# Optimization experiments

Measured on AMD Instinct MI355X. Metric: run time of the kernel, lower is better.

## Reference

```python
import jax, jax.numpy as jnp
import numpy as np

N_NODES = 100000
N_EDGES = 1600000
N_GRAPHS = 64
D_IN, D_HID, D_LAT = 2, 64, 32


def setup_inputs() -> dict:
    key = jax.random.key(0)
    k1, k2, k3, k4, k5, k6, k7 = jax.random.split(key, 7)
    x = jax.random.normal(k1, (N_NODES, D_IN), dtype=jnp.float32)
    edge_index = jax.random.randint(k2, (2, N_EDGES), 0, N_NODES, dtype=jnp.int64)
    batch = jnp.sort(jax.random.randint(k3, (N_NODES,), 0, N_GRAPHS, dtype=jnp.int64))
    # GCNConv params (glorot-ish scale)
    W1 = jax.random.normal(k4, (D_IN, D_HID), dtype=jnp.float32) * (1.0 / np.sqrt(D_IN))
    b1 = jnp.zeros((D_HID,), dtype=jnp.float32)
    W2 = jax.random.normal(k5, (D_HID, D_LAT), dtype=jnp.float32) * (1.0 / np.sqrt(D_HID))
    b2 = jnp.zeros((D_LAT,), dtype=jnp.float32)
    return {"x": x, "W1": W1, "b1": b1, "W2": W2, "b2": b2,
            "edge_index": edge_index, "batch": batch}


def _gcn_conv(x, W, b, src, dst, n_nodes):
    """PyG GCNConv: add self-loops, symmetric deg^-1/2 normalization, linear, scatter-add."""
    h = x @ W  # [N, d_out]
    loop = jnp.arange(n_nodes, dtype=src.dtype)
    src_f = jnp.concatenate([src, loop])
    dst_f = jnp.concatenate([dst, loop])
    deg = jax.ops.segment_sum(jnp.ones_like(dst_f, dtype=h.dtype), dst_f,
                              num_segments=n_nodes)  # in-degree incl. self-loop
    dis = jnp.where(deg > 0, jax.lax.rsqrt(deg), 0.0)
    norm = dis[src_f] * dis[dst_f]  # [E+N]
    msg = h[src_f] * norm[:, None]  # edge gather (memory-bound)
    out = jax.ops.segment_sum(msg, dst_f, num_segments=n_nodes)
    return out + b


def reference(x, W1, b1, W2, b2, edge_index, batch):
    src, dst = edge_index[0], edge_index[1]
    n = x.shape[0]
    h = jax.nn.relu(_gcn_conv(x, W1, b1, src, dst, n))
    z = _gcn_conv(h, W2, b2, src, dst, n)
    # global_mean_pool over graph ids
    sums = jax.ops.segment_sum(z, batch, num_segments=N_GRAPHS)
    cnts = jax.ops.segment_sum(jnp.ones((n,), dtype=z.dtype), batch,
                               num_segments=N_GRAPHS)
    return sums / jnp.maximum(cnts, 1.0)[:, None]
```

## Files before the change

kernel.cpp:

```cpp
#include <hip/hip_runtime.h>
#include <hip/hip_fp16.h>

#define N_NODES  100000
#define N_EDGES  1600000
#define N_GRAPHS 64
#define NBUCK    391
#define NBLK     256
#define CHUNK    (N_EDGES / NBLK)
#define NODEBLK  1563

#define OFF_GSTART 0
#define OFF_ROWPTR 128
#define OFF_DIS    100224
#define OFF_S      200320
#define OFF_CSR    400384
#define OFF_Q      2000384
#define OFF_BHIST  2000384
#define OFF_BOFFL  2100736
#define OFF_BSUM   2201088
#define OFF_BSTART 2201600
#define OFF_TMP    2202112

typedef float fvec2 __attribute__((ext_vector_type(2)));

__device__ __forceinline__ int excl_scan_256(int v, int* wsum) {
  int t = threadIdx.x, lane = t & 63, w = t >> 6;
  int x = v;
#pragma unroll
  for (int off = 1; off < 64; off <<= 1) {
    int y = __shfl_up(x, off, 64);
    if (lane >= off) x += y;
  }
  if (lane == 63) wsum[w] = x;
  __syncthreads();
  if (t == 0) {
    int r = 0;
#pragma unroll
    for (int i = 0; i < 4; ++i) { int tv = wsum[i]; wsum[i] = r; r += tv; }
  }
  __syncthreads();
  return x - v + wsum[w];
}

__device__ __forceinline__ int excl_scan_512(int v, int* wsum) {
  int t = threadIdx.x, lane = t & 63, w = t >> 6;
  int x = v;
#pragma unroll
  for (int off = 1; off < 64; off <<= 1) {
    int y = __shfl_up(x, off, 64);
    if (lane >= off) x += y;
  }
  if (lane == 63) wsum[w] = x;
  __syncthreads();
  if (t == 0) {
    int r = 0;
#pragma unroll
    for (int i = 0; i < 8; ++i) { int tv = wsum[i]; wsum[i] = r; r += tv; }
  }
  __syncthreads();
  return x - v + wsum[w];
}

__global__ void k_hist(const int* __restrict__ dst, int* __restrict__ bhist) {
  __shared__ int hist[NBUCK];
  int t = threadIdx.x, k = blockIdx.x;
  for (int b = t; b < NBUCK; b += 256) hist[b] = 0;
  __syncthreads();
  int e0 = k * CHUNK, e1 = e0 + CHUNK;
  for (int e = e0 + t; e < e1; e += 256) atomicAdd(&hist[dst[e] >> 8], 1);
  __syncthreads();
  for (int b = t; b < NBUCK; b += 256) bhist[b * NBLK + k] = hist[b];
}

__global__ void k_scan_a(const int* __restrict__ bhist, int* __restrict__ boffl,
                         int* __restrict__ bsum, const int* __restrict__ batch,
                         int* __restrict__ gstart) {
  __shared__ int wsum[4];
  int t = threadIdx.x, b = blockIdx.x;
  int i = b * 256 + t;
  if (i < N_NODES) {
    int bi = batch[i];
    if (i == 0) {
      for (int g = 0; g <= bi; ++g) gstart[g] = 0;
    } else {
      int bp = batch[i - 1];
      for (int g = bp + 1; g <= bi; ++g) gstart[g] = i;
    }
    if (i == N_NODES - 1) {
      for (int g = bi + 1; g <= N_GRAPHS; ++g) gstart[g] = N_NODES;
    }
  }
  int v = bhist[b * NBLK + t];
  int ex = excl_scan_256(v, wsum);
  boffl[b * NBLK + t] = ex;
  if (t == NBLK - 1) bsum[b] = ex + v;
}

__global__ void k_scan_b(const int* __restrict__ bsum, int* __restrict__ bstart,
                         float* __restrict__ pooled) {
  __shared__ int wsum[8];
  int t = threadIdx.x;
  for (int i = t; i < N_GRAPHS * 32; i += 512) pooled[i] = 0.f;
  int v = (t < NBUCK) ? bsum[t] : 0;
  int ex = excl_scan_512(v, wsum);
  if (t <= NBUCK) bstart[t] = ex;
}

__global__ void k_scatter(const int* __restrict__ src, const int* __restrict__ dst,
                          const int* __restrict__ bstart, const int* __restrict__ boffl,
                          int* __restrict__ tmp) {
  __shared__ int sbase[NBUCK];
  __shared__ int fill[NBUCK];
  int t = threadIdx.x, k = blockIdx.x;
  for (int b = t; b < NBUCK; b += 256) {
    sbase[b] = bstart[b] + boffl[b * NBLK + k];
    fill[b] = 0;
  }
  __syncthreads();
  int e0 = k * CHUNK, e1 = e0 + CHUNK;
  for (int e = e0 + t; e < e1; e += 256) {
    int s_ = src[e], d_ = dst[e];
    int b = d_ >> 8;
    int pos = sbase[b] + atomicAdd(&fill[b], 1);
    tmp[pos] = (s_ << 8) | (d_ & 255);
  }
}

__global__ void k_fine(const int* __restrict__ tmp, const int* __restrict__ bstart,
                       const float* __restrict__ x, int* __restrict__ csr_src,
                       int* __restrict__ row_ptr, float* __restrict__ dis,
                       float2* __restrict__ s) {
  __shared__ int hist[256];
  __shared__ int fill[256];
  __shared__ int wsum[4];
  int t = threadIdx.x, b = blockIdx.x;
  int base_n = b << 8;
  int e0 = bstart[b], e1 = bstart[b + 1];
  hist[t] = 0;
  __syncthreads();
  for (int e = e0 + t; e < e1; e += 256) atomicAdd(&hist[tmp[e] & 255], 1);
  __syncthreads();
  int h = hist[t];
  int ex = excl_scan_256(h, wsum);
  hist[t] = ex;
  fill[t] = 0;
  int nn = min(256, N_NODES - base_n);
  if (t < nn) {
    int v = base_n + t;
    row_ptr[v] = e0 + ex;
    float dv = rsqrtf((float)(h + 1));
    dis[v] = dv;
    float2 xv = ((const float2*)x)[v];
    s[v] = make_float2(xv.x * dv, xv.y * dv);
  }
  if (b == NBUCK - 1 && t == 0) row_ptr[N_NODES] = e1;
  __syncthreads();
  for (int e = e0 + t; e < e1; e += 256) {
    int p = tmp[e];
    int fine = p & 255;
    int pos = e0 + hist[fine] + atomicAdd(&fill[fine], 1);
    csr_src[pos] = p >> 8;
  }
}

__global__ void __launch_bounds__(64)
k_layer1(const float2* __restrict__ s, const int* __restrict__ row_ptr,
         const int* __restrict__ csr_src, const float* __restrict__ W1,
         const float* __restrict__ b1, const float* __restrict__ W2,
         int4* __restrict__ q8) {
  __shared__ float4 sWB[64];
  __shared__ float4 sW2[512];
  int t = threadIdx.x;
  sWB[t] = make_float4(W1[t], W1[64 + t], b1[t], 0.f);
#pragma unroll
  for (int i = 0; i < 8; ++i) sW2[i * 64 + t] = ((const float4*)W2)[i * 64 + t];
  __syncthreads();
  int base = blockIdx.x * 128;
  int vA = base + t, vB = base + 64 + t;
  bool okA = vA < N_NODES, okB = vB < N_NODES;
  float tA0 = 0.f, tA1 = 0.f, tB0 = 0.f, tB1 = 0.f, dA = 0.f, dB = 0.f;
  if (okA) {
    int beg = row_ptr[vA], end = row_ptr[vA + 1];
    float2 sv = s[vA];
    tA0 = sv.x; tA1 = sv.y;
    int k = beg;
    for (; k + 4 <= end; k += 4) {
      float2 a = s[csr_src[k]], b = s[csr_src[k + 1]];
      float2 c = s[csr_src[k + 2]], d = s[csr_src[k + 3]];
      tA0 += (a.x + b.x) + (c.x + d.x);
      tA1 += (a.y + b.y) + (c.y + d.y);
    }
    for (; k < end; ++k) { float2 su = s[csr_src[k]]; tA0 += su.x; tA1 += su.y; }
    dA = rsqrtf((float)(end - beg + 1));
    tA0 *= dA; tA1 *= dA;
  }
  if (okB) {
    int beg = row_ptr[vB], end = row_ptr[vB + 1];
    float2 sv = s[vB];
    tB0 = sv.x; tB1 = sv.y;
    int k = beg;
    for (; k + 4 <= end; k += 4) {
      float2 a = s[csr_src[k]], b = s[csr_src[k + 1]];
      float2 c = s[csr_src[k + 2]], d = s[csr_src[k + 3]];
      tB0 += (a.x + b.x) + (c.x + d.x);
      tB1 += (a.y + b.y) + (c.y + d.y);
    }
    for (; k < end; ++k) { float2 su = s[csr_src[k]]; tB0 += su.x; tB1 += su.y; }
    dB = rsqrtf((float)(end - beg + 1));
    tB0 *= dB; tB1 *= dB;
  }
  float4 aA[8], aB[8];
#pragma unroll
  for (int m = 0; m < 8; ++m) {
    aA[m] = make_float4(0.f, 0.f, 0.f, 0.f);
    aB[m] = make_float4(0.f, 0.f, 0.f, 0.f);
  }
  for (int j = 0; j < 64; ++j) {
    float4 wb = sWB[j];
    float rA = fmaxf(fmaf(tA0, wb.x, fmaf(tA1, wb.y, wb.z)), 0.f);
    float rB = fmaxf(fmaf(tB0, wb.x, fmaf(tB1, wb.y, wb.z)), 0.f);
#pragma unroll
    for (int m = 0; m < 8; ++m) {
      float4 w = sW2[j * 8 + m];
      aA[m].x = fmaf(rA, w.x, aA[m].x);
      aA[m].y = fmaf(rA, w.y, aA[m].y);
      aA[m].z = fmaf(rA, w.z, aA[m].z);
      aA[m].w = fmaf(rA, w.w, aA[m].w);
      aB[m].x = fmaf(rB, w.x, aB[m].x);
      aB[m].y = fmaf(rB, w.y, aB[m].y);
      aB[m].z = fmaf(rB, w.z, aB[m].z);
      aB[m].w = fmaf(rB, w.w, aB[m].w);
    }
  }
  if (okA) {
    int pk[8];
#pragma unroll
    for (int m = 0; m < 8; ++m) {
      int wrd = __builtin_amdgcn_cvt_pk_fp8_f32(aA[m].x * dA, aA[m].y * dA, 0, false);
      wrd = __builtin_amdgcn_cvt_pk_fp8_f32(aA[m].z * dA, aA[m].w * dA, wrd, true);
      pk[m] = wrd;
    }
    q8[vA * 2]     = make_int4(pk[0], pk[1], pk[2], pk[3]);
    q8[vA * 2 + 1] = make_int4(pk[4], pk[5], pk[6], pk[7]);
  }
  if (okB) {
    int pk[8];
#pragma unroll
    for (int m = 0; m < 8; ++m) {
      int wrd = __builtin_amdgcn_cvt_pk_fp8_f32(aB[m].x * dB, aB[m].y * dB, 0, false);
      wrd = __builtin_amdgcn_cvt_pk_fp8_f32(aB[m].z * dB, aB[m].w * dB, wrd, true);
      pk[m] = wrd;
    }
    q8[vB * 2]     = make_int4(pk[0], pk[1], pk[2], pk[3]);
    q8[vB * 2 + 1] = make_int4(pk[4], pk[5], pk[6], pk[7]);
  }
}

__device__ __forceinline__ float4 qdec(unsigned int d) {
  fvec2 lo = __builtin_amdgcn_cvt_pk_f32_fp8(d, false);
  fvec2 hi = __builtin_amdgcn_cvt_pk_f32_fp8(d, true);
  return make_float4(lo.x, lo.y, hi.x, hi.y);
}

__global__ void k_layer2(const unsigned int* __restrict__ q, const float* __restrict__ dis,
                         const int* __restrict__ row_ptr, const int* __restrict__ csr_src,
                         const int* __restrict__ batch, float* __restrict__ pooled) {
  __shared__ float4 red[32][9];
  int t = threadIdx.x;
  int fp = t & 7;
  int rg = t >> 3;
  int vb = blockIdx.x * 64;
  int nlast = min(vb + 63, N_NODES - 1);
  bool uniform = (batch[vb] == batch[nlast]);
  int v0 = vb + rg * 2;
  int v1 = min(v0 + 2, N_NODES);
  float4 acc = make_float4(0.f, 0.f, 0.f, 0.f);
  int curg = (v0 < N_NODES) ? batch[v0] : -1;
  for (int v = v0; v < v1; ++v) {
    if (!uniform) {
      int g = batch[v];
      if (g != curg) {
        int base = curg * 32 + fp * 4;
        atomicAdd(&pooled[base],     acc.x);
        atomicAdd(&pooled[base + 1], acc.y);
        atomicAdd(&pooled[base + 2], acc.z);
        atomicAdd(&pooled[base + 3], acc.w);
        acc = make_float4(0.f, 0.f, 0.f, 0.f);
        curg = g;
      }
    }
    int e0 = row_ptr[v], e1 = row_ptr[v + 1];
    float4 z = qdec(q[v * 8 + fp]);
    int k = e0;
    for (; k + 8 <= e1; k += 8) {
      int u0 = csr_src[k],     u1 = csr_src[k + 1], u2 = csr_src[k + 2], u3 = csr_src[k + 3];
      int u4 = csr_src[k + 4], u5 = csr_src[k + 5], u6 = csr_src[k + 6], u7 = csr_src[k + 7];
      float4 f0 = qdec(q[u0 * 8 + fp]);
      float4 f1 = qdec(q[u1 * 8 + fp]);
      float4 f2 = qdec(q[u2 * 8 + fp]);
      float4 f3 = qdec(q[u3 * 8 + fp]);
      float4 f4 = qdec(q[u4 * 8 + fp]);
      float4 f5 = qdec(q[u5 * 8 + fp]);
      float4 f6 = qdec(q[u6 * 8 + fp]);
      float4 f7 = qdec(q[u7 * 8 + fp]);
      z.x += ((f0.x + f1.x) + (f2.x + f3.x)) + ((f4.x + f5.x) + (f6.x + f7.x));
      z.y += ((f0.y + f1.y) + (f2.y + f3.y)) + ((f4.y + f5.y) + (f6.y + f7.y));
      z.z += ((f0.z + f1.z) + (f2.z + f3.z)) + ((f4.z + f5.z) + (f6.z + f7.z));
      z.w += ((f0.w + f1.w) + (f2.w + f3.w)) + ((f4.w + f5.w) + (f6.w + f7.w));
    }
    for (; k < e1; ++k) {
      float4 f = qdec(q[csr_src[k] * 8 + fp]);
      z.x += f.x; z.y += f.y; z.z += f.z; z.w += f.w;
    }
    float dvv = dis[v];
    acc.x = fmaf(z.x, dvv, acc.x);
    acc.y = fmaf(z.y, dvv, acc.y);
    acc.z = fmaf(z.z, dvv, acc.z);
    acc.w = fmaf(z.w, dvv, acc.w);
  }
  if (uniform) {
    red[rg][fp] = acc;
    __syncthreads();
    if (t < 8) {
      float4 ssum = make_float4(0.f, 0.f, 0.f, 0.f);
#pragma unroll
      for (int r = 0; r < 32; ++r) {
        float4 x4 = red[r][t];
        ssum.x += x4.x; ssum.y += x4.y; ssum.z += x4.z; ssum.w += x4.w;
      }
      int gg = batch[vb];
      int base = gg * 32 + t * 4;
      atomicAdd(&pooled[base],     ssum.x);
      atomicAdd(&pooled[base + 1], ssum.y);
      atomicAdd(&pooled[base + 2], ssum.z);
      atomicAdd(&pooled[base + 3], ssum.w);
    }
  } else if (v0 < N_NODES) {
    int base = curg * 32 + fp * 4;
    atomicAdd(&pooled[base],     acc.x);
    atomicAdd(&pooled[base + 1], acc.y);
    atomicAdd(&pooled[base + 2], acc.z);
    atomicAdd(&pooled[base + 3], acc.w);
  }
}

__global__ void k_final(float* __restrict__ out, const int* __restrict__ gstart,
                        const float* __restrict__ b2) {
  int i = blockIdx.x * 256 + threadIdx.x;
  if (i < N_GRAPHS * 32) {
    int g = i >> 5, l = i & 31;
    int c = gstart[g + 1] - gstart[g];
    out[i] = (c > 0) ? out[i] / (float)c + b2[l] : 0.f;
  }
}

extern "C" void kernel_launch(void* const* d_in, const int* in_sizes, int n_in,
                              void* d_out, int out_size, void* d_ws, size_t ws_size,
                              hipStream_t stream) {
  (void)in_sizes; (void)n_in; (void)out_size; (void)ws_size;
  const float* x   = (const float*)d_in[0];
  const float* W1  = (const float*)d_in[1];
  const float* b1  = (const float*)d_in[2];
  const float* W2  = (const float*)d_in[3];
  const float* b2  = (const float*)d_in[4];
  const int* edge  = (const int*)d_in[5];
  const int* batch = (const int*)d_in[6];
  const int* src = edge;
  const int* dst = edge + N_EDGES;
  float* out = (float*)d_out;

  int* ws      = (int*)d_ws;
  int* gstart  = ws + OFF_GSTART;
  int* row_ptr = ws + OFF_ROWPTR;
  float* dis   = (float*)(ws + OFF_DIS);
  float2* s    = (float2*)(ws + OFF_S);
  int* csr_src = ws + OFF_CSR;
  int4* q8     = (int4*)(ws + OFF_Q);
  int* bhist   = ws + OFF_BHIST;
  int* boffl   = ws + OFF_BOFFL;
  int* bsum    = ws + OFF_BSUM;
  int* bstart  = ws + OFF_BSTART;
  int* tmp     = ws + OFF_TMP;

  k_hist<<<NBLK, 256, 0, stream>>>(dst, bhist);
  k_scan_a<<<NBUCK, 256, 0, stream>>>(bhist, boffl, bsum, batch, gstart);
  k_scan_b<<<1, 512, 0, stream>>>(bsum, bstart, out);
  k_scatter<<<NBLK, 256, 0, stream>>>(src, dst, bstart, boffl, tmp);
  k_fine<<<NBUCK, 256, 0, stream>>>(tmp, bstart, x, csr_src, row_ptr, dis, s);
  k_layer1<<<(N_NODES + 127) / 128, 64, 0, stream>>>(s, row_ptr, csr_src,
                                                     W1, b1, W2, q8);
  k_layer2<<<NODEBLK, 256, 0, stream>>>((const unsigned int*)q8, dis, row_ptr,
                                        csr_src, batch, out);
  k_final<<<8, 256, 0, stream>>>(out, gstart, b2);
}
```

Baseline: 96.43 us.

## Stage scatter and fine-sort in LDS to coalesce global writes

k_scatter now locally sorts each block's edge chunk into an LDS buffer by bucket, then writes each bucket's contiguous run to global memory. This replaces the random single-int global writes. k_fine likewise loads a bucket's edges into LDS, builds the CSR order in LDS and writes it out contiguously, with a global fallback when a bucket exceeds capacity. Both kernels use more LDS, which lowers occupancy, and the scan helpers gain an extra barrier so wsum can be reused safely.

```diff
diff --git a/kernel.cpp b/kernel.cpp
--- a/kernel.cpp
+++ b/kernel.cpp
@@ -8,6 +8,7 @@
 #define NBLK     256
 #define CHUNK    (N_EDGES / NBLK)
 #define NODEBLK  1563
+#define FCAP     6144
 
 #define OFF_GSTART 0
 #define OFF_ROWPTR 128
@@ -39,7 +40,9 @@
     for (int i = 0; i < 4; ++i) { int tv = wsum[i]; wsum[i] = r; r += tv; }
   }
   __syncthreads();
-  return x - v + wsum[w];
+  int res = x - v + wsum[w];
+  __syncthreads();
+  return res;
 }
 
 __device__ __forceinline__ int excl_scan_512(int v, int* wsum) {
@@ -58,7 +61,9 @@
     for (int i = 0; i < 8; ++i) { int tv = wsum[i]; wsum[i] = r; r += tv; }
   }
   __syncthreads();
-  return x - v + wsum[w];
+  int res = x - v + wsum[w];
+  __syncthreads();
+  return res;
 }
 
 __global__ void k_hist(const int* __restrict__ dst, int* __restrict__ bhist) {
@@ -108,21 +113,48 @@
 
 __global__ void k_scatter(const int* __restrict__ src, const int* __restrict__ dst,
                           const int* __restrict__ bstart, const int* __restrict__ boffl,
-                          int* __restrict__ tmp) {
-  __shared__ int sbase[NBUCK];
+                          const int* __restrict__ bhist, int* __restrict__ tmp) {
+  __shared__ int ebuf[CHUNK];
+  __shared__ int loff[NBUCK];
   __shared__ int fill[NBUCK];
+  __shared__ int gbase[NBUCK];
+  __shared__ int wsum[4];
+  __shared__ int tot0sh;
   int t = threadIdx.x, k = blockIdx.x;
-  for (int b = t; b < NBUCK; b += 256) {
-    sbase[b] = bstart[b] + boffl[b * NBLK + k];
-    fill[b] = 0;
+  int c0 = bhist[t * NBLK + k];
+  int ex0 = excl_scan_256(c0, wsum);
+  loff[t] = ex0;
+  fill[t] = 0;
+  gbase[t] = bstart[t] + boffl[t * NBLK + k];
+  if (t == 255) tot0sh = ex0 + c0;
+  __syncthreads();
+  int idx = 256 + t;
+  int c1 = (idx < NBUCK) ? bhist[idx * NBLK + k] : 0;
+  int ex1 = excl_scan_256(c1, wsum);
+  if (idx < NBUCK) {
+    loff[idx] = tot0sh + ex1;
+    fill[idx] = 0;
+    gbase[idx] = bstart[idx] + boffl[idx * NBLK + k];
   }
   __syncthreads();
   int e0 = k * CHUNK, e1 = e0 + CHUNK;
   for (int e = e0 + t; e < e1; e += 256) {
     int s_ = src[e], d_ = dst[e];
     int b = d_ >> 8;
-    int pos = sbase[b] + atomicAdd(&fill[b], 1);
-    tmp[pos] = (s_ << 8) | (d_ & 255);
+    int pos = loff[b] + atomicAdd(&fill[b], 1);
+    ebuf[pos] = (s_ << 8) | (d_ & 255);
+  }
+  __syncthreads();
+  int wv = t >> 6;
+  int sub = (t >> 4) & 3;
+  int off0 = t & 15;
+  const int ngroups = (NBUCK + 3) / 4;
+  for (int g = wv; g < ngroups; g += 4) {
+    int b = g * 4 + sub;
+    if (b < NBUCK) {
+      int len = fill[b], lb = loff[b], gb = gbase[b];
+      for (int o = off0; o < len; o += 16) tmp[gb + o] = ebuf[lb + o];
+    }
   }
 }
 
@@ -130,15 +162,27 @@
                        const float* __restrict__ x, int* __restrict__ csr_src,
                        int* __restrict__ row_ptr, float* __restrict__ dis,
                        float2* __restrict__ s) {
+  __shared__ int ebuf[FCAP];
+  __shared__ int csrbuf[FCAP];
   __shared__ int hist[256];
   __shared__ int fill[256];
   __shared__ int wsum[4];
   int t = threadIdx.x, b = blockIdx.x;
   int base_n = b << 8;
   int e0 = bstart[b], e1 = bstart[b + 1];
+  int cnt = e1 - e0;
+  bool lds_path = (cnt <= FCAP);
   hist[t] = 0;
   __syncthreads();
-  for (int e = e0 + t; e < e1; e += 256) atomicAdd(&hist[tmp[e] & 255], 1);
+  if (lds_path) {
+    for (int i = t; i < cnt; i += 256) {
+      int p = tmp[e0 + i];
+      ebuf[i] = p;
+      atomicAdd(&hist[p & 255], 1);
+    }
+  } else {
+    for (int e = e0 + t; e < e1; e += 256) atomicAdd(&hist[tmp[e] & 255], 1);
+  }
   __syncthreads();
   int h = hist[t];
   int ex = excl_scan_256(h, wsum);
@@ -155,11 +199,22 @@
   }
   if (b == NBUCK - 1 && t == 0) row_ptr[N_NODES] = e1;
   __syncthreads();
-  for (int e = e0 + t; e < e1; e += 256) {
-    int p = tmp[e];
-    int fine = p & 255;
-    int pos = e0 + hist[fine] + atomicAdd(&fill[fine], 1);
-    csr_src[pos] = p >> 8;
+  if (lds_path) {
+    for (int i = t; i < cnt; i += 256) {
+      int p = ebuf[i];
+      int fine = p & 255;
+      int pos = hist[fine] + atomicAdd(&fill[fine], 1);
+      csrbuf[pos] = p >> 8;
+    }
+    __syncthreads();
+    for (int i = t; i < cnt; i += 256) csr_src[e0 + i] = csrbuf[i];
+  } else {
+    for (int e = e0 + t; e < e1; e += 256) {
+      int p = tmp[e];
+      int fine = p & 255;
+      int pos = e0 + hist[fine] + atomicAdd(&fill[fine], 1);
+      csr_src[pos] = p >> 8;
+    }
   }
 }
 
@@ -385,7 +440,7 @@
   k_hist<<<NBLK, 256, 0, stream>>>(dst, bhist);
   k_scan_a<<<NBUCK, 256, 0, stream>>>(bhist, boffl, bsum, batch, gstart);
   k_scan_b<<<1, 512, 0, stream>>>(bsum, bstart, out);
-  k_scatter<<<NBLK, 256, 0, stream>>>(src, dst, bstart, boffl, tmp);
+  k_scatter<<<NBLK, 256, 0, stream>>>(src, dst, bstart, boffl, bhist, tmp);
   k_fine<<<NBUCK, 256, 0, stream>>>(tmp, bstart, x, csr_src, row_ptr, dis, s);
   k_layer1<<<(N_NODES + 127) / 128, 64, 0, stream>>>(s, row_ptr, csr_src,
                                                      W1, b1, W2, q8);
```

Measured after the change: 100.5 us. 1.04x slower.
